# Kernel optimization log

Hardware: AMD Instinct MI355X
Metric: run time of the kernel (lower is better)

The kernel has to match this reference:

```python
import jax, jax.numpy as jnp
import numpy as np

B, DIN, H, DOUT = 2048, 1024, 2048, 1024
N_WIDTH, N_ROUTED = 8, 4  # n_layers - 2 = 4 routed expert layers
BN_EPS = 1e-5


def setup_inputs() -> dict:
    key = jax.random.key(0)
    ks = jax.random.split(key, 8)
    # kaiming-normal-ish scales
    x = jax.random.normal(ks[0], (B, DIN), dtype=jnp.float32)
    start_W = jax.random.normal(ks[1], (DIN, H), dtype=jnp.float32) * np.sqrt(2.0 / DIN)
    start_b = jnp.zeros((H,), jnp.float32)
    start_gamma = jnp.ones((H,), jnp.float32)
    start_beta = jnp.zeros((H,), jnp.float32)
    expert_W = jax.random.normal(ks[2], (N_ROUTED, N_WIDTH, H, H), dtype=jnp.float32) * np.sqrt(2.0 / H)
    expert_b = jnp.zeros((N_ROUTED, N_WIDTH, H), jnp.float32)
    bn_gamma = jnp.ones((N_ROUTED, H), jnp.float32)
    bn_beta = jnp.zeros((N_ROUTED, H), jnp.float32)
    dqn_W = jax.random.normal(ks[3], (H, N_WIDTH), dtype=jnp.float32) * np.sqrt(1.0 / H)
    dqn_b = jnp.zeros((N_WIDTH,), jnp.float32)
    end_W = jax.random.normal(ks[4], (H, DOUT), dtype=jnp.float32) * np.sqrt(2.0 / H)
    end_b = jnp.zeros((DOUT,), jnp.float32)
    return {"x": x, "start_W": start_W, "start_b": start_b,
            "start_gamma": start_gamma, "start_beta": start_beta,
            "expert_W": expert_W, "expert_b": expert_b,
            "bn_gamma": bn_gamma, "bn_beta": bn_beta,
            "dqn_W": dqn_W, "dqn_b": dqn_b,
            "end_W": end_W, "end_b": end_b}


def _batchnorm(h, gamma, beta):
    # training-mode BatchNorm1d: biased variance over batch axis
    mu = h.mean(0)
    var = jnp.mean((h - mu) ** 2, axis=0)
    return gamma * (h - mu) * jax.lax.rsqrt(var + BN_EPS) + beta


def reference(x, start_W, start_b, start_gamma, start_beta,
              expert_W, expert_b, bn_gamma, bn_beta,
              dqn_W, dqn_b, end_W, end_b):
    # start: Linear + ReLU + BatchNorm1d
    h = jax.nn.relu(x @ start_W + start_b)            # [B, H]
    h = _batchnorm(h, start_gamma, start_beta)
    # routed expert layers (eval mode: deterministic argmax routing, eps=-1)
    for i in range(N_ROUTED):
        logits = h @ dqn_W + dqn_b                    # [B, E]
        actions = jnp.argmax(logits, axis=1)          # [B]
        onehot = jax.nn.one_hot(actions, N_WIDTH, dtype=h.dtype)  # [B, E]
        # compute all experts densely, then select per-sample expert
        y_all = jax.nn.relu(jnp.einsum('bi,eio->beo', h, expert_W[i]) + expert_b[i][None])  # [B, E, H]
        h = jnp.einsum('beo,be->bo', y_all, onehot)   # [B, H]
        h = _batchnorm(h, bn_gamma[i], bn_beta[i])
    # end: Linear + ReLU
    return jax.nn.relu(h @ end_W + end_b)             # [B, DOUT]
```

## Files before the change

### kernel.cpp

```cpp
#include <hip/hip_runtime.h>
#include <math.h>

#define B_SZ 2048
#define DIN  1024
#define H    2048
#define DOUT 1024
#define NEXP 8
#define NL   4

typedef _Float16 f16;
typedef _Float16 f16x4 __attribute__((ext_vector_type(4)));
typedef _Float16 f16x8 __attribute__((ext_vector_type(8)));
typedef float    f32x4 __attribute__((ext_vector_type(4)));

#define MFMA16(a,b,c) __builtin_amdgcn_mfma_f32_16x16x32_f16((a),(b),(c),0,0,0)

__global__ __launch_bounds__(256) void k_convert(const float* __restrict__ x,
                                                 f16* __restrict__ hi, f16* __restrict__ lo, int n4){
  int stride = gridDim.x * blockDim.x;
  for (int i = blockIdx.x*blockDim.x + threadIdx.x; i < n4; i += stride){
    float4 v = ((const float4*)x)[i];
    f16 h0=(f16)v.x, h1=(f16)v.y, h2=(f16)v.z, h3=(f16)v.w;
    f16x4 hv = {h0,h1,h2,h3};
    f16x4 lv = {(f16)((v.x-(float)h0)*2048.0f),(f16)((v.y-(float)h1)*2048.0f),
                (f16)((v.z-(float)h2)*2048.0f),(f16)((v.w-(float)h3)*2048.0f)};
    ((f16x4*)hi)[i] = hv;
    ((f16x4*)lo)[i] = lv;
  }
}

template<int PRECISE>
__global__ __launch_bounds__(256, 2) void k_gemm(
    const f16* __restrict__ Ahi, const f16* __restrict__ Alo, int lda,
    const float* __restrict__ Wbase, const float* __restrict__ biasBase,
    int K, int N, int M,
    float* __restrict__ Cout, int ldc,
    const int* __restrict__ row_idx, const int* __restrict__ offsets,
    const int* __restrict__ tile_map, const int* __restrict__ ntiles,
    int wStride, int bStride)
{
  const bool ident = (tile_map == nullptr);
  int e, mt, roff, cnt;
  if (!ident){
    int ti = blockIdx.y;
    if (ti >= *ntiles) return;
    int mv = tile_map[ti]; e = mv >> 16; mt = mv & 0xffff;
    roff = offsets[e]; cnt = offsets[e+1] - roff;
  } else { e = 0; mt = blockIdx.y; roff = 0; cnt = M; }

  const float* W    = Wbase   + (size_t)e * wStride;
  const float* bias = biasBase+ (size_t)e * bStride;
  const int n0   = blockIdx.x * 128;
  const int tid  = threadIdx.x;
  const int lane = tid & 63;
  const int wid  = tid >> 6;
  const int wm   = (wid >> 1) * 64;
  const int wn   = (wid & 1) * 64;

  __shared__ f16x8 sAh[128*5];
  __shared__ f16x8 sAl[PRECISE ? 128*5 : 1];
  __shared__ f16x8 sBh[128*5];
  __shared__ f16x8 sBl[PRECISE ? 128*5 : 1];

  const int r1 = tid >> 2, sl = tid & 3, r2 = r1 + 64;
  int gr1, gr2;
  {
    int i1 = mt*128 + r1, i2 = mt*128 + r2;
    if (ident){ gr1 = i1; gr2 = i2; }
    else { gr1 = row_idx[roff + (i1 < cnt ? i1 : 0)];
           gr2 = row_idx[roff + (i2 < cnt ? i2 : 0)]; }
  }
  const f16* a1h = Ahi + (size_t)gr1*lda + sl*8;
  const f16* a2h = Ahi + (size_t)gr2*lda + sl*8;
  const f16 *a1l = nullptr, *a2l = nullptr;
  if constexpr (PRECISE){
    a1l = Alo + (size_t)gr1*lda + sl*8;
    a2l = Alo + (size_t)gr2*lda + sl*8;
  }

  const int bn = tid & 127, kb = tid >> 7;
  const float* wp0 = W + (size_t)(kb*16) * N + n0 + bn;

  f32x4 acc0[4][4] = {};
  f32x4 acc1[4][4] = {};

  for (int k0 = 0; k0 < K; k0 += 32){
    __syncthreads();
    sAh[r1*5 + sl] = *(const f16x8*)(a1h + k0);
    sAh[r2*5 + sl] = *(const f16x8*)(a2h + k0);
    if constexpr (PRECISE){
      sAl[r1*5 + sl] = *(const f16x8*)(a1l + k0);
      sAl[r2*5 + sl] = *(const f16x8*)(a2l + k0);
    }
    {
      const float* wp = wp0 + (size_t)k0 * N;
      f16 hs[16], ls[16];
      #pragma unroll
      for (int i = 0; i < 16; i++){
        float w = wp[(size_t)i * N] * 16.0f;
        f16 wh = (f16)w; hs[i] = wh;
        if constexpr (PRECISE) ls[i] = (f16)((w - (float)wh) * 2048.0f);
      }
      f16x8 v0 = {hs[0],hs[1],hs[2],hs[3],hs[4],hs[5],hs[6],hs[7]};
      f16x8 v1 = {hs[8],hs[9],hs[10],hs[11],hs[12],hs[13],hs[14],hs[15]};
      sBh[bn*5 + kb*2 + 0] = v0;
      sBh[bn*5 + kb*2 + 1] = v1;
      if constexpr (PRECISE){
        f16x8 u0 = {ls[0],ls[1],ls[2],ls[3],ls[4],ls[5],ls[6],ls[7]};
        f16x8 u1 = {ls[8],ls[9],ls[10],ls[11],ls[12],ls[13],ls[14],ls[15]};
        sBl[bn*5 + kb*2 + 0] = u0;
        sBl[bn*5 + kb*2 + 1] = u1;
      }
    }
    __syncthreads();

    f16x8 ah[4], al[4];
    #pragma unroll
    for (int mf = 0; mf < 4; mf++){
      int row = wm + mf*16 + (lane & 15);
      ah[mf] = sAh[row*5 + (lane >> 4)];
      if constexpr (PRECISE) al[mf] = sAl[row*5 + (lane >> 4)];
    }
    #pragma unroll
    for (int nf = 0; nf < 4; nf++){
      int col = wn + nf*16 + (lane & 15);
      f16x8 bh = sBh[col*5 + (lane >> 4)];
      f16x8 bl;
      if constexpr (PRECISE) bl = sBl[col*5 + (lane >> 4)];
      #pragma unroll
      for (int mf = 0; mf < 4; mf++){
        acc0[mf][nf] = MFMA16(ah[mf], bh, acc0[mf][nf]);
        if constexpr (PRECISE){
          acc1[mf][nf] = MFMA16(ah[mf], bl, acc1[mf][nf]);
          acc1[mf][nf] = MFMA16(al[mf], bh, acc1[mf][nf]);
        }
      }
    }
  }

  const float s1 = 1.0f/16.0f, s2 = 1.0f/(16.0f*2048.0f);
  float bvs[4];
  #pragma unroll
  for (int nf = 0; nf < 4; nf++) bvs[nf] = bias[n0 + wn + nf*16 + (lane & 15)];
  #pragma unroll
  for (int mf = 0; mf < 4; mf++){
    #pragma unroll
    for (int j = 0; j < 4; j++){
      int rt   = wm + mf*16 + (lane >> 4)*4 + j;
      int ridx = mt*128 + rt;
      int gr; bool valid;
      if (ident){ gr = ridx; valid = true; }
      else { valid = (ridx < cnt); gr = valid ? row_idx[roff + ridx] : 0; }
      if (valid){
        float* cp = Cout + (size_t)gr*ldc + n0 + wn + (lane & 15);
        #pragma unroll
        for (int nf = 0; nf < 4; nf++){
          float v = acc0[mf][nf][j]*s1 + bvs[nf];
          if constexpr (PRECISE) v += acc1[mf][nf][j]*s2;
          v = v > 0.0f ? v : 0.0f;
          cp[nf*16] = v;
        }
      }
    }
  }
}

__global__ __launch_bounds__(256) void k_stats(const float* __restrict__ P,
                                               float* __restrict__ psum, float* __restrict__ psq){
  int c  = blockIdx.x*64 + (threadIdx.x & 63);
  int rs = threadIdx.x >> 6;
  int r0 = blockIdx.y * 256;
  float s = 0.f, q = 0.f;
  for (int r = r0 + rs; r < r0 + 256; r += 4){
    float v = P[(size_t)r*H + c]; s += v; q += v*v;
  }
  __shared__ float ls[4][64], lq[4][64];
  ls[rs][threadIdx.x & 63] = s; lq[rs][threadIdx.x & 63] = q;
  __syncthreads();
  if (threadIdx.x < 64){
    int cc = threadIdx.x;
    float S = ls[0][cc]+ls[1][cc]+ls[2][cc]+ls[3][cc];
    float Q = lq[0][cc]+lq[1][cc]+lq[2][cc]+lq[3][cc];
    psum[(size_t)blockIdx.y*H + blockIdx.x*64 + cc] = S;
    psq [(size_t)blockIdx.y*H + blockIdx.x*64 + cc] = Q;
  }
}

__global__ __launch_bounds__(256) void k_norm(const float* __restrict__ P,
    const float* __restrict__ psum, const float* __restrict__ psq,
    const float* __restrict__ gamma, const float* __restrict__ beta,
    f16* __restrict__ Hhi, f16* __restrict__ Hlo){
  __shared__ float sS[64], sT[64];
  int c0 = blockIdx.x * 64;
  int tid = threadIdx.x;
  if (tid < 64){
    float s = 0.f, q = 0.f;
    #pragma unroll
    for (int j = 0; j < 8; j++){ s += psum[(size_t)j*H + c0 + tid]; q += psq[(size_t)j*H + c0 + tid]; }
    float mu  = s * (1.0f/B_SZ);
    float var = q * (1.0f/B_SZ) - mu*mu; var = var > 0.f ? var : 0.f;
    float r   = 1.0f / sqrtf(var + 1e-5f);
    float g   = gamma[c0 + tid] * r;
    sS[tid] = g; sT[tid] = beta[c0 + tid] - mu*g;
  }
  __syncthreads();
  int cg = (tid & 15) * 4;
  int r0 = blockIdx.y * 256;
  for (int r = r0 + (tid >> 4); r < r0 + 256; r += 16){
    float4 v = *(const float4*)&P[(size_t)r*H + c0 + cg];
    float h0 = v.x*sS[cg]   + sT[cg];
    float h1 = v.y*sS[cg+1] + sT[cg+1];
    float h2 = v.z*sS[cg+2] + sT[cg+2];
    float h3 = v.w*sS[cg+3] + sT[cg+3];
    f16 a0=(f16)h0, a1=(f16)h1, a2=(f16)h2, a3=(f16)h3;
    f16x4 hv = {a0,a1,a2,a3};
    f16x4 lv = {(f16)((h0-(float)a0)*2048.0f),(f16)((h1-(float)a1)*2048.0f),
                (f16)((h2-(float)a2)*2048.0f),(f16)((h3-(float)a3)*2048.0f)};
    *(f16x4*)&Hhi[(size_t)r*H + c0 + cg] = hv;
    *(f16x4*)&Hlo[(size_t)r*H + c0 + cg] = lv;
  }
}

__global__ __launch_bounds__(256) void k_logits(const f16* __restrict__ Hhi, const f16* __restrict__ Hlo,
    const float* __restrict__ dqnW, const float* __restrict__ dqnB, int* __restrict__ actions){
  int row  = blockIdx.x*4 + (threadIdx.x >> 6);
  int lane = threadIdx.x & 63;
  float acc[8] = {0,0,0,0,0,0,0,0};
  const f16* ph = Hhi + (size_t)row*H;
  const f16* pl = Hlo + (size_t)row*H;
  for (int k = lane; k < H; k += 64){
    float h = (float)ph[k] + (float)pl[k]*(1.0f/2048.0f);
    const float* w = dqnW + (size_t)k*NEXP;
    float4 w0 = *(const float4*)w;
    float4 w1 = *(const float4*)(w+4);
    acc[0] += h*w0.x; acc[1] += h*w0.y; acc[2] += h*w0.z; acc[3] += h*w0.w;
    acc[4] += h*w1.x; acc[5] += h*w1.y; acc[6] += h*w1.z; acc[7] += h*w1.w;
  }
  #pragma unroll
  for (int off = 32; off; off >>= 1){
    #pragma unroll
    for (int e2 = 0; e2 < 8; e2++) acc[e2] += __shfl_down(acc[e2], off);
  }
  if (lane == 0){
    float best = acc[0] + dqnB[0]; int bi = 0;
    #pragma unroll
    for (int e2 = 1; e2 < 8; e2++){ float v = acc[e2] + dqnB[e2]; if (v > best){ best = v; bi = e2; } }
    actions[row] = bi;
  }
}

__global__ __launch_bounds__(256) void k_route(const int* __restrict__ actions, int* __restrict__ offsets,
    int* __restrict__ row_idx, int* __restrict__ tile_map, int* __restrict__ ntiles){
  __shared__ int cnt[8], cur[8];
  int tid = threadIdx.x;
  if (tid < 8) cnt[tid] = 0;
  __syncthreads();
  for (int b = tid; b < B_SZ; b += 256) atomicAdd(&cnt[actions[b]], 1);
  __syncthreads();
  if (tid == 0){
    int o = 0, nt = 0;
    for (int e2 = 0; e2 < 8; e2++){
      offsets[e2] = o; cur[e2] = o;
      int c = cnt[e2];
      int t = (c + 127) >> 7;
      for (int ti = 0; ti < t; ti++) tile_map[nt++] = (e2 << 16) | ti;
      o += c;
    }
    offsets[8] = o;
    *ntiles = nt;
  }
  __syncthreads();
  for (int b = tid; b < B_SZ; b += 256){
    int a = actions[b];
    int p = atomicAdd(&cur[a], 1);
    row_idx[p] = b;
  }
}

extern "C" void kernel_launch(void* const* d_in, const int* in_sizes, int n_in,
                              void* d_out, int out_size, void* d_ws, size_t ws_size,
                              hipStream_t stream){
  const float* x           = (const float*)d_in[0];
  const float* start_W     = (const float*)d_in[1];
  const float* start_b     = (const float*)d_in[2];
  const float* start_gamma = (const float*)d_in[3];
  const float* start_beta  = (const float*)d_in[4];
  const float* expert_W    = (const float*)d_in[5];
  const float* expert_b    = (const float*)d_in[6];
  const float* bn_gamma    = (const float*)d_in[7];
  const float* bn_beta     = (const float*)d_in[8];
  const float* dqn_W       = (const float*)d_in[9];
  const float* dqn_b       = (const float*)d_in[10];
  const float* end_W       = (const float*)d_in[11];
  const float* end_b       = (const float*)d_in[12];
  float* out = (float*)d_out;

  char* ws = (char*)d_ws;
  size_t off = 0;
  auto alloc = [&](size_t bytes){ void* p = ws + off; off += (bytes + 255) & ~(size_t)255; return p; };
  f16*   Hhi     = (f16*)  alloc((size_t)B_SZ*H*2);
  f16*   Hlo     = (f16*)  alloc((size_t)B_SZ*H*2);
  float* Ppre    = (float*)alloc((size_t)B_SZ*H*4);
  float* psum    = (float*)alloc((size_t)8*H*4);
  float* psq     = (float*)alloc((size_t)8*H*4);
  int*   actions = (int*)  alloc(B_SZ*4);
  int*   row_idx = (int*)  alloc(B_SZ*4);
  int*   offsets = (int*)  alloc(16*4);
  int*   tile_map= (int*)  alloc(32*4);
  int*   ntiles  = (int*)  alloc(64);

  k_convert<<<512, 256, 0, stream>>>(x, Hhi, Hlo, B_SZ*DIN/4);
  k_gemm<1><<<dim3(H/128, B_SZ/128), 256, 0, stream>>>(
      Hhi, Hlo, DIN, start_W, start_b, DIN, H, B_SZ, Ppre, H,
      nullptr, nullptr, nullptr, nullptr, 0, 0);
  k_stats<<<dim3(H/64, 8), 256, 0, stream>>>(Ppre, psum, psq);
  k_norm <<<dim3(H/64, 8), 256, 0, stream>>>(Ppre, psum, psq, start_gamma, start_beta, Hhi, Hlo);

  for (int i = 0; i < NL; i++){
    k_logits<<<B_SZ/4, 256, 0, stream>>>(Hhi, Hlo, dqn_W, dqn_b, actions);
    k_route <<<1, 256, 0, stream>>>(actions, offsets, row_idx, tile_map, ntiles);
    const float* Wb = expert_W + (size_t)i*NEXP*H*H;
    const float* bb = expert_b + (size_t)i*NEXP*H;
    if (i < 3)
      k_gemm<1><<<dim3(H/128, 23), 256, 0, stream>>>(
          Hhi, Hlo, H, Wb, bb, H, H, B_SZ, Ppre, H,
          row_idx, offsets, tile_map, ntiles, H*H, H);
    else
      k_gemm<0><<<dim3(H/128, 23), 256, 0, stream>>>(
          Hhi, nullptr, H, Wb, bb, H, H, B_SZ, Ppre, H,
          row_idx, offsets, tile_map, ntiles, H*H, H);
    k_stats<<<dim3(H/64, 8), 256, 0, stream>>>(Ppre, psum, psq);
    k_norm <<<dim3(H/64, 8), 256, 0, stream>>>(Ppre, psum, psq,
        bn_gamma + (size_t)i*H, bn_beta + (size_t)i*H, Hhi, Hlo);
  }

  k_gemm<0><<<dim3(DOUT/128, B_SZ/128), 256, 0, stream>>>(
      Hhi, nullptr, H, end_W, end_b, H, DOUT, B_SZ, out, DOUT,
      nullptr, nullptr, nullptr, nullptr, 0, 0);
}
```

Before: 799.4 us.

## Prefetch next K-tile into registers in GEMM, vectorize logits loads

The GEMM main loop now issues the global loads for the next K step into registers right after the shared-memory stores, so the load latency overlaps the MFMA work of the current step. An extra barrier is added at the end of each iteration. The fp32-to-fp16 weight split now uses packed round-toward-zero conversion (cvt_pkrtz), which changes the rounding mode of the hi/lo split. The logits kernel reads 8 halves per lane with vector loads instead of scalar loads. The register prefetch raises register pressure and may lower occupancy.

```diff
diff --git a/kernel.cpp b/kernel.cpp
--- a/kernel.cpp
+++ b/kernel.cpp
@@ -11,6 +11,7 @@
 typedef _Float16 f16;
 typedef _Float16 f16x4 __attribute__((ext_vector_type(4)));
 typedef _Float16 f16x8 __attribute__((ext_vector_type(8)));
+typedef __fp16   h16x2 __attribute__((ext_vector_type(2)));
 typedef float    f32x4 __attribute__((ext_vector_type(4)));
 
 #define MFMA16(a,b,c) __builtin_amdgcn_mfma_f32_16x16x32_f16((a),(b),(c),0,0,0)
@@ -84,22 +85,43 @@
   f32x4 acc0[4][4] = {};
   f32x4 acc1[4][4] = {};
 
+  f16x8 rA1h, rA2h, rA1l, rA2l;
+  float rW[16];
+
+  auto issue = [&](int kk){
+    rA1h = *(const f16x8*)(a1h + kk);
+    rA2h = *(const f16x8*)(a2h + kk);
+    if constexpr (PRECISE){
+      rA1l = *(const f16x8*)(a1l + kk);
+      rA2l = *(const f16x8*)(a2l + kk);
+    }
+    const float* wp = wp0 + (size_t)kk * N;
+    #pragma unroll
+    for (int i = 0; i < 16; i++) rW[i] = wp[(size_t)i * N];
+  };
+
+  issue(0);
+
   for (int k0 = 0; k0 < K; k0 += 32){
-    __syncthreads();
-    sAh[r1*5 + sl] = *(const f16x8*)(a1h + k0);
-    sAh[r2*5 + sl] = *(const f16x8*)(a2h + k0);
+    sAh[r1*5 + sl] = rA1h;
+    sAh[r2*5 + sl] = rA2h;
     if constexpr (PRECISE){
-      sAl[r1*5 + sl] = *(const f16x8*)(a1l + k0);
-      sAl[r2*5 + sl] = *(const f16x8*)(a2l + k0);
+      sAl[r1*5 + sl] = rA1l;
+      sAl[r2*5 + sl] = rA2l;
     }
     {
-      const float* wp = wp0 + (size_t)k0 * N;
       f16 hs[16], ls[16];
       #pragma unroll
-      for (int i = 0; i < 16; i++){
-        float w = wp[(size_t)i * N] * 16.0f;
-        f16 wh = (f16)w; hs[i] = wh;
-        if constexpr (PRECISE) ls[i] = (f16)((w - (float)wh) * 2048.0f);
+      for (int i = 0; i < 16; i += 2){
+        float w0 = rW[i]   * 16.0f;
+        float w1 = rW[i+1] * 16.0f;
+        h16x2 hp = __builtin_amdgcn_cvt_pkrtz(w0, w1);
+        hs[i] = (f16)hp.x; hs[i+1] = (f16)hp.y;
+        if constexpr (PRECISE){
+          h16x2 lp = __builtin_amdgcn_cvt_pkrtz((w0-(float)hp.x)*2048.0f,
+                                                (w1-(float)hp.y)*2048.0f);
+          ls[i] = (f16)lp.x; ls[i+1] = (f16)lp.y;
+        }
       }
       f16x8 v0 = {hs[0],hs[1],hs[2],hs[3],hs[4],hs[5],hs[6],hs[7]};
       f16x8 v1 = {hs[8],hs[9],hs[10],hs[11],hs[12],hs[13],hs[14],hs[15]};
@@ -113,6 +135,8 @@
       }
     }
     __syncthreads();
+
+    if (k0 + 32 < K) issue(k0 + 32);
 
     f16x8 ah[4], al[4];
     #pragma unroll
@@ -136,6 +160,7 @@
         }
       }
     }
+    __syncthreads();
   }
 
   const float s1 = 1.0f/16.0f, s2 = 1.0f/(16.0f*2048.0f);
@@ -228,13 +253,20 @@
   float acc[8] = {0,0,0,0,0,0,0,0};
   const f16* ph = Hhi + (size_t)row*H;
   const f16* pl = Hlo + (size_t)row*H;
-  for (int k = lane; k < H; k += 64){
-    float h = (float)ph[k] + (float)pl[k]*(1.0f/2048.0f);
-    const float* w = dqnW + (size_t)k*NEXP;
-    float4 w0 = *(const float4*)w;
-    float4 w1 = *(const float4*)(w+4);
-    acc[0] += h*w0.x; acc[1] += h*w0.y; acc[2] += h*w0.z; acc[3] += h*w0.w;
-    acc[4] += h*w1.x; acc[5] += h*w1.y; acc[6] += h*w1.z; acc[7] += h*w1.w;
+  #pragma unroll
+  for (int t = 0; t < 4; t++){
+    int k = t*512 + lane*8;
+    f16x8 h8 = *(const f16x8*)(ph + k);
+    f16x8 l8 = *(const f16x8*)(pl + k);
+    #pragma unroll
+    for (int j = 0; j < 8; j++){
+      float h = (float)h8[j] + (float)l8[j]*(1.0f/2048.0f);
+      const float* w = dqnW + (size_t)(k+j)*NEXP;
+      float4 w0 = *(const float4*)w;
+      float4 w1 = *(const float4*)(w+4);
+      acc[0] += h*w0.x; acc[1] += h*w0.y; acc[2] += h*w0.z; acc[3] += h*w0.w;
+      acc[4] += h*w1.x; acc[5] += h*w1.y; acc[6] += h*w1.z; acc[7] += h*w1.w;
+    }
   }
   #pragma unroll
   for (int off = 32; off; off >>= 1){
```

Result: faster. 755.3 us (-5.5%).
